# Kernel optimization log

Hardware: AMD Instinct MI355X
Metric: run time of the kernel (lower is better)

The kernel has to match this reference:

```python
import jax, jax.numpy as jnp
import numpy as np

BATCH, SEQ, FEAT, UNITS, OUT = 128, 2048, 64, 64, 6


def setup_inputs() -> dict:
    key = jax.random.key(0)
    ks = jax.random.split(key, 12)
    s = 0.05
    inp = {
        "x": jax.random.normal(ks[0], (BATCH, SEQ, FEAT), dtype=jnp.float32),
        # LSTMCell 0 (kernel, recurrent_kernel, bias); gate order i,f,g,o
        "W0": jax.random.normal(ks[1], (FEAT, 4 * UNITS), dtype=jnp.float32) * s,
        "U0": jax.random.normal(ks[2], (UNITS, 4 * UNITS), dtype=jnp.float32) * s,
        "b0": jax.random.normal(ks[3], (4 * UNITS,), dtype=jnp.float32) * s,
        # LSTMCell 1 (shared by layers 2 AND 3, as in the original code)
        "W1": jax.random.normal(ks[4], (UNITS, 4 * UNITS), dtype=jnp.float32) * s,
        "U1": jax.random.normal(ks[5], (UNITS, 4 * UNITS), dtype=jnp.float32) * s,
        "b1": jax.random.normal(ks[6], (4 * UNITS,), dtype=jnp.float32) * s,
        # Dense heads
        "Wf": jax.random.normal(ks[7], (UNITS, 64), dtype=jnp.float32) * s,
        "bf": jax.random.normal(ks[8], (64,), dtype=jnp.float32) * s,
        "Wo": jax.random.normal(ks[9], (64, OUT), dtype=jnp.float32) * s,
        "bo": jax.random.normal(ks[10], (OUT,), dtype=jnp.float32) * s,
    }
    return inp


def _lstm_cell(c, h, xin, W, U, b):
    # Keras LSTMCell math, gate order i, f, g(candidate), o
    z = xin @ W + h @ U + b  # [B, 4U]
    i, f, g, o = jnp.split(z, 4, axis=-1)
    c_new = jax.nn.sigmoid(f) * c + jax.nn.sigmoid(i) * jnp.tanh(g)
    h_new = jax.nn.sigmoid(o) * jnp.tanh(c_new)
    return c_new, h_new


def reference(x, W0, U0, b0, W1, U1, b1, Wf, bf, Wo, bo):
    B = x.shape[0]
    z = jnp.zeros((B, UNITS), dtype=x.dtype)
    init = (z, z, z, z, z, z)  # (c0,h0,c1,h1,c2,h2)

    def step(carry, xt):
        c0, h0, c1, h1, c2, h2 = carry
        c0, h0 = _lstm_cell(c0, h0, xt, W0, U0, b0)
        c1, h1 = _lstm_cell(c1, h1, h0, W1, U1, b1)
        # NOTE: original code reuses rnn_cell1's weights for the 3rd layer
        c2, h2 = _lstm_cell(c2, h2, h1, W1, U1, b1)
        return (c0, h0, c1, h1, c2, h2), None

    xt = jnp.swapaxes(x, 0, 1)  # [T, B, F]
    (c0, h0, c1, h1, c2, h2), _ = jax.lax.scan(step, init, xt)
    y = jax.nn.relu(h2 @ Wf + bf)
    return y @ Wo + bo
```

## Files before the change

### kernel.cpp

```cpp
#include <hip/hip_runtime.h>

#define BATCHN 128
#define SEQT   2048
#define FEAT   64
#define UNITS  64
#define NCOL   256
#define OUTD   6

typedef __fp16 hv2 __attribute__((ext_vector_type(2)));

__device__ __forceinline__ float fast_exp2(float x) {
#if __has_builtin(__builtin_amdgcn_exp2f)
    return __builtin_amdgcn_exp2f(x);
#else
    return exp2f(x);
#endif
}
__device__ __forceinline__ float fast_rcp(float x) {
#if __has_builtin(__builtin_amdgcn_rcpf)
    return __builtin_amdgcn_rcpf(x);
#else
    return 1.0f / x;
#endif
}
__device__ __forceinline__ float sig_(float x) {
    return fast_rcp(1.0f + fast_exp2(-1.4426950408889634f * x));
}
__device__ __forceinline__ float tanh_(float x) {
    float e = fast_exp2(-2.8853900817779268f * x);
    return fmaf(2.0f, fast_rcp(1.0f + e), -1.0f);
}

__device__ __forceinline__ float fdot2_(hv2 a, hv2 b, float c) {
#if __has_builtin(__builtin_amdgcn_fdot2)
    return __builtin_amdgcn_fdot2(a, b, c, false);
#else
    return fmaf((float)a.x, (float)b.x, fmaf((float)a.y, (float)b.y, c));
#endif
}
__device__ __forceinline__ hv2 cvtpk_(float a, float b) {
    return __builtin_amdgcn_cvt_pkrtz(a, b);
}
__device__ __forceinline__ unsigned int rlane_(unsigned int v, int l) {
    return (unsigned int)__builtin_amdgcn_readlane((int)v, l);
}
__device__ __forceinline__ float bperm_(int byteaddr, float v) {
    return __builtin_bit_cast(float,
        __builtin_amdgcn_ds_bpermute(byteaddr, __builtin_bit_cast(int, v)));
}

__global__ __launch_bounds__(384, 1)
void lstm3_ffrec2(const float* __restrict__ x,
                  const float* __restrict__ W0, const float* __restrict__ U0,
                  const float* __restrict__ b0,
                  const float* __restrict__ W1, const float* __restrict__ U1,
                  const float* __restrict__ b1,
                  const float* __restrict__ Wf, const float* __restrict__ bfv,
                  const float* __restrict__ Wo, const float* __restrict__ bov,
                  float* __restrict__ out)
{
    const int b   = blockIdx.x;
    const int tid = threadIdx.x;
    const int wid = tid >> 6;
    const int g   = wid >> 1;
    const int r   = wid & 1;
    const int u   = tid & 63;
    const int j32 = u & 31;

    __shared__ unsigned int lhp[3][2][32];
    __shared__ __align__(16) float lzf[3][2][UNITS][4];
    __shared__ float lh2f[UNITS];
    __shared__ float lact[UNITS];

    const float* M = (g == 0) ? ((r == 0) ? W0 : U0) : ((r == 0) ? W1 : U1);
    const float* bsel = (g == 0) ? b0 : b1;

    hv2 wM[32][4];
    float biasv[4];
#pragma unroll
    for (int gg = 0; gg < 4; ++gg) {
        const int col = (gg << 6) + u;
#pragma unroll
        for (int j = 0; j < 32; ++j) {
            hv2 w;
            w.x = (__fp16)M[(2 * j) * NCOL + col];
            w.y = (__fp16)M[(2 * j + 1) * NCOL + col];
            wM[j][gg] = w;
        }
        biasv[gg] = bsel[col];
    }

    if (tid < 192) ((unsigned int*)lhp)[tid] = 0u;
    for (int i = tid; i < 3 * 2 * UNITS * 4; i += 384) ((float*)lzf)[i] = 0.f;

    const float2* x2 = (const float2*)(x + (size_t)b * SEQT * FEAT);
    float2 xrA = {0.f, 0.f}, xrB = {0.f, 0.f};
    if (wid == 0 && u < 32) {
        xrA = x2[0 * 32 + u];
        xrB = x2[1 * 32 + u];
    }
    __syncthreads();

    const int alpha = 2 * g + r;
    float c = 0.f, h = 0.f;
    unsigned int rpk = 0u;

#define TICK(TK, XR)                                                          \
    {                                                                         \
        const int t_ = (TK) - alpha;                                          \
        const float2 xcur = XR;                                               \
        if (wid == 0 && u < 32) {                    \
            int tn = (TK) + 2; if (tn > SEQT - 1) tn = SEQT - 1;              \
            XR = x2[(size_t)tn * 32 + u];                                     \
        }                                                                     \
        if (t_ >= 0 && t_ < SEQT) {                                           \
            const int p_ = t_ & 1;                                            \
            unsigned int srcpk;                                               \
            float4 zin = {0.f, 0.f, 0.f, 0.f};                                \
            if (r == 0) {                                                     \
                srcpk = (g == 0) ? __builtin_bit_cast(unsigned int,           \
                                                      cvtpk_(xcur.x, xcur.y)) \
                                 : lhp[g - 1][p_][j32];            \
            } else {                                                          \
                srcpk = rpk;                                                  \
                zin = *(const float4*)&lzf[g][p_][u][0];     \
            }                                                                 \
            float aA0 = 0.f, aA1 = 0.f, aA2 = 0.f, aA3 = 0.f;                 \
            float aB0 = 0.f, aB1 = 0.f, aB2 = 0.f, aB3 = 0.f;                 \
            _Pragma("unroll")                                                 \
            for (int j = 0; j < 32; j += 2) {                                 \
                hv2 p0 = __builtin_bit_cast(hv2, rlane_(srcpk, j));           \
                hv2 p1 = __builtin_bit_cast(hv2, rlane_(srcpk, j + 1));       \
                aA0 = fdot2_(p0, wM[j][0], aA0);                              \
                aA1 = fdot2_(p0, wM[j][1], aA1);                              \
                aA2 = fdot2_(p0, wM[j][2], aA2);                              \
                aA3 = fdot2_(p0, wM[j][3], aA3);                              \
                aB0 = fdot2_(p1, wM[j + 1][0], aB0);                          \
                aB1 = fdot2_(p1, wM[j + 1][1], aB1);                          \
                aB2 = fdot2_(p1, wM[j + 1][2], aB2);                          \
                aB3 = fdot2_(p1, wM[j + 1][3], aB3);                          \
            }                                                                 \
            if (r == 0) {                   \
                float4 z4 = {aA0 + aB0 + biasv[0], aA1 + aB1 + biasv[1],      \
                             aA2 + aB2 + biasv[2], aA3 + aB3 + biasv[3]};     \
                *(float4*)&lzf[g][p_][u][0] = z4;                             \
            } else {                       \
                const float zi = aA0 + aB0 + zin.x;                           \
                const float zf = aA1 + aB1 + zin.y;                           \
                const float zg = aA2 + aB2 + zin.z;                           \
                const float zo = aA3 + aB3 + zin.w;                           \
                const float ig = sig_(zi), fg = sig_(zf);                     \
                const float gv = tanh_(zg), og = sig_(zo);                    \
                c = fg * c + ig * gv;                                         \
                h = og * tanh_(c);                                            \
                const float h0 = bperm_(j32 * 8,     h);                      \
                const float h1 = bperm_(j32 * 8 + 4, h);                      \
                rpk = __builtin_bit_cast(unsigned int, cvtpk_(h0, h1));       \
                if (u < 32) lhp[g][p_][u] = rpk;                              \
                if (g == 2 && t_ == SEQT - 1) lh2f[u] = h;                    \
            }                                                                 \
        }                                                                     \
        asm volatile("s_waitcnt lgkmcnt(0)\n\ts_barrier" ::: "memory");       \
    }

    for (int tk = 0; tk < SEQT + 6; tk += 2) {
        TICK(tk,     xrA)
        TICK(tk + 1, xrB)
    }
#undef TICK

    __syncthreads();

    if (tid < UNITS) {
        float a = bfv[tid];
#pragma unroll
        for (int k = 0; k < UNITS; ++k) a += lh2f[k] * Wf[k * 64 + tid];
        lact[tid] = fmaxf(a, 0.f);
    }
    __syncthreads();
    if (tid < OUTD) {
        float a = bov[tid];
#pragma unroll
        for (int k = 0; k < UNITS; ++k) a += lact[k] * Wo[k * OUTD + tid];
        out[b * OUTD + tid] = a;
    }
}

extern "C" void kernel_launch(void* const* d_in, const int* in_sizes, int n_in,
                              void* d_out, int out_size, void* d_ws, size_t ws_size,
                              hipStream_t stream) {
    const float* x   = (const float*)d_in[0];
    const float* W0  = (const float*)d_in[1];
    const float* U0  = (const float*)d_in[2];
    const float* b0  = (const float*)d_in[3];
    const float* W1  = (const float*)d_in[4];
    const float* U1  = (const float*)d_in[5];
    const float* b1  = (const float*)d_in[6];
    const float* Wf  = (const float*)d_in[7];
    const float* bfv = (const float*)d_in[8];
    const float* Wo  = (const float*)d_in[9];
    const float* bov = (const float*)d_in[10];
    float* out = (float*)d_out;

    lstm3_ffrec2<<<BATCHN, 384, 0, stream>>>(x, W0, U0, b0, W1, U1, b1,
                                             Wf, bfv, Wo, bov, out);
}
```

Baseline: 1.898 ms.

## Process two timesteps per pipeline tick to halve block barriers

Restructures the wavefront-pipelined LSTM so each tick advances two consecutive timesteps instead of one. This halves the number of workgroup barriers and LDS handoffs. Input-projection waves now compute two projections per tick into double-buffered LDS slots. Recurrent waves run two dependent cell updates back-to-back, using direct readlane of fp32 h for the inner step. The trade-off is a longer serial critical path per tick on the recurrent waves and extra readlane/pack instructions.

```diff
diff --git a/kernel.cpp b/kernel.cpp
--- a/kernel.cpp
+++ b/kernel.cpp
@@ -6,6 +6,7 @@
 #define UNITS  64
 #define NCOL   256
 #define OUTD   6
+#define NTICK  1030
 
 typedef __fp16 hv2 __attribute__((ext_vector_type(2)));
 
@@ -44,20 +45,27 @@
 __device__ __forceinline__ unsigned int rlane_(unsigned int v, int l) {
     return (unsigned int)__builtin_amdgcn_readlane((int)v, l);
 }
+__device__ __forceinline__ float rlf_(float v, int l) {
+    return __builtin_bit_cast(float,
+        __builtin_amdgcn_readlane(__builtin_bit_cast(int, v), l));
+}
 __device__ __forceinline__ float bperm_(int byteaddr, float v) {
     return __builtin_bit_cast(float,
         __builtin_amdgcn_ds_bpermute(byteaddr, __builtin_bit_cast(int, v)));
 }
+__device__ __forceinline__ unsigned int pku_(hv2 v) {
+    return __builtin_bit_cast(unsigned int, v);
+}
 
 __global__ __launch_bounds__(384, 1)
-void lstm3_ffrec2(const float* __restrict__ x,
-                  const float* __restrict__ W0, const float* __restrict__ U0,
-                  const float* __restrict__ b0,
-                  const float* __restrict__ W1, const float* __restrict__ U1,
-                  const float* __restrict__ b1,
-                  const float* __restrict__ Wf, const float* __restrict__ bfv,
-                  const float* __restrict__ Wo, const float* __restrict__ bov,
-                  float* __restrict__ out)
+void lstm3_2step(const float* __restrict__ x,
+                 const float* __restrict__ W0, const float* __restrict__ U0,
+                 const float* __restrict__ b0,
+                 const float* __restrict__ W1, const float* __restrict__ U1,
+                 const float* __restrict__ b1,
+                 const float* __restrict__ Wf, const float* __restrict__ bfv,
+                 const float* __restrict__ Wo, const float* __restrict__ bov,
+                 float* __restrict__ out)
 {
     const int b   = blockIdx.x;
     const int tid = threadIdx.x;
@@ -67,8 +75,8 @@
     const int u   = tid & 63;
     const int j32 = u & 31;
 
-    __shared__ unsigned int lhp[3][2][32];
-    __shared__ __align__(16) float lzf[3][2][UNITS][4];
+    __shared__ unsigned int lhp[3][2][2][32];
+    __shared__ __align__(16) float lzf[3][2][2][UNITS][4];
     __shared__ float lh2f[UNITS];
     __shared__ float lact[UNITS];
 
@@ -90,84 +98,135 @@
         biasv[gg] = bsel[col];
     }
 
-    if (tid < 192) ((unsigned int*)lhp)[tid] = 0u;
-    for (int i = tid; i < 3 * 2 * UNITS * 4; i += 384) ((float*)lzf)[i] = 0.f;
+    if (tid < 384) ((unsigned int*)lhp)[tid] = 0u;
+    for (int i = tid; i < 3 * 2 * 2 * UNITS * 4; i += 384) ((float*)lzf)[i] = 0.f;
 
     const float2* x2 = (const float2*)(x + (size_t)b * SEQT * FEAT);
-    float2 xrA = {0.f, 0.f}, xrB = {0.f, 0.f};
+    float2 xA0 = {0.f,0.f}, xA1 = {0.f,0.f}, xB0 = {0.f,0.f}, xB1 = {0.f,0.f};
     if (wid == 0 && u < 32) {
-        xrA = x2[0 * 32 + u];
-        xrB = x2[1 * 32 + u];
+        xA0 = x2[0 * 32 + u];  xA1 = x2[1 * 32 + u];
+        xB0 = x2[2 * 32 + u];  xB1 = x2[3 * 32 + u];
     }
     __syncthreads();
 
     const int alpha = 2 * g + r;
-    float c = 0.f, h = 0.f;
+    float c = 0.f;
     unsigned int rpk = 0u;
 
-#define TICK(TK, XR)                                                          \
-    {                                                                         \
-        const int t_ = (TK) - alpha;                                          \
-        const float2 xcur = XR;                                               \
-        if (wid == 0 && u < 32) {                    \
-            int tn = (TK) + 2; if (tn > SEQT - 1) tn = SEQT - 1;              \
-            XR = x2[(size_t)tn * 32 + u];                                     \
-        }                                                                     \
-        if (t_ >= 0 && t_ < SEQT) {                                           \
-            const int p_ = t_ & 1;                                            \
-            unsigned int srcpk;                                               \
-            float4 zin = {0.f, 0.f, 0.f, 0.f};                                \
+#define DOT_PK(SRC, S0, S1, S2, S3)                                           \
+    {                                                                         \
+        float dA0=0.f,dA1=0.f,dA2=0.f,dA3=0.f,dB0=0.f,dB1=0.f,dB2=0.f,dB3=0.f;\
+        _Pragma("unroll")                                                     \
+        for (int j = 0; j < 32; j += 2) {                                     \
+            hv2 p0 = __builtin_bit_cast(hv2, rlane_(SRC, j));                 \
+            hv2 p1 = __builtin_bit_cast(hv2, rlane_(SRC, j + 1));             \
+            dA0 = fdot2_(p0, wM[j][0], dA0);                                  \
+            dA1 = fdot2_(p0, wM[j][1], dA1);                                  \
+            dA2 = fdot2_(p0, wM[j][2], dA2);                                  \
+            dA3 = fdot2_(p0, wM[j][3], dA3);                                  \
+            dB0 = fdot2_(p1, wM[j + 1][0], dB0);                              \
+            dB1 = fdot2_(p1, wM[j + 1][1], dB1);                              \
+            dB2 = fdot2_(p1, wM[j + 1][2], dB2);                              \
+            dB3 = fdot2_(p1, wM[j + 1][3], dB3);                              \
+        }                                                                     \
+        S0 = dA0 + dB0; S1 = dA1 + dB1; S2 = dA2 + dB2; S3 = dA3 + dB3;       \
+    }
+
+#define DOT_H(HV, S0, S1, S2, S3)                                             \
+    {                                                                         \
+        float dA0=0.f,dA1=0.f,dA2=0.f,dA3=0.f,dB0=0.f,dB1=0.f,dB2=0.f,dB3=0.f;\
+        _Pragma("unroll")                                                     \
+        for (int j = 0; j < 32; j += 2) {                                     \
+            hv2 p0 = cvtpk_(rlf_(HV, 2 * j),     rlf_(HV, 2 * j + 1));        \
+            hv2 p1 = cvtpk_(rlf_(HV, 2 * j + 2), rlf_(HV, 2 * j + 3));        \
+            dA0 = fdot2_(p0, wM[j][0], dA0);                                  \
+            dA1 = fdot2_(p0, wM[j][1], dA1);                                  \
+            dA2 = fdot2_(p0, wM[j][2], dA2);                                  \
+            dA3 = fdot2_(p0, wM[j][3], dA3);                                  \
+            dB0 = fdot2_(p1, wM[j + 1][0], dB0);                              \
+            dB1 = fdot2_(p1, wM[j + 1][1], dB1);                              \
+            dB2 = fdot2_(p1, wM[j + 1][2], dB2);                              \
+            dB3 = fdot2_(p1, wM[j + 1][3], dB3);                              \
+        }                                                                     \
+        S0 = dA0 + dB0; S1 = dA1 + dB1; S2 = dA2 + dB2; S3 = dA3 + dB3;       \
+    }
+
+#define GATES(Z0, Z1, Z2, Z3, HOUT)                                           \
+    {                                                                         \
+        const float ig = sig_(Z0), fg = sig_(Z1);                             \
+        const float gv = tanh_(Z2), og = sig_(Z3);                            \
+        c = fg * c + ig * gv;                                                 \
+        HOUT = og * tanh_(c);                                                 \
+    }
+
+#define TICK(TK, X0, X1)                                                      \
+    {                                                                         \
+        const int t0_ = 2 * ((TK) - alpha);                                   \
+        const float2 xc0 = X0, xc1 = X1;                                      \
+        if (wid == 0 && u < 32) {        \
+            int tn = 2 * ((TK) + 2);                                          \
+            if (tn > SEQT - 2) tn = SEQT - 2;                                 \
+            X0 = x2[(size_t)tn * 32 + u];                                     \
+            X1 = x2[(size_t)(tn + 1) * 32 + u];                               \
+        }                                                                     \
+        if (t0_ >= 0 && t0_ < SEQT) {                                         \
+            const int q_ = (TK) & 1;                                          \
             if (r == 0) {                                                     \
-                srcpk = (g == 0) ? __builtin_bit_cast(unsigned int,           \
-                                                      cvtpk_(xcur.x, xcur.y)) \
-                                 : lhp[g - 1][p_][j32];            \
+                unsigned int fp0, fp1;                                        \
+                if (g == 0) {                                                 \
+                    fp0 = pku_(cvtpk_(xc0.x, xc0.y));                         \
+                    fp1 = pku_(cvtpk_(xc1.x, xc1.y));                         \
+                } else {                                                      \
+                    fp0 = lhp[g - 1][q_ ^ 1][0][j32];                         \
+                    fp1 = lhp[g - 1][q_ ^ 1][1][j32];                         \
+                }                                                             \
+                float s0, s1, s2, s3;                                         \
+                DOT_PK(fp0, s0, s1, s2, s3)                                   \
+                {                                                             \
+                    float4 z4 = {s0 + biasv[0], s1 + biasv[1],                \
+                                 s2 + biasv[2], s3 + biasv[3]};               \
+                    *(float4*)&lzf[g][q_][0][u][0] = z4;                      \
+                }                                                             \
+                DOT_PK(fp1, s0, s1, s2, s3)                                   \
+                {                                                             \
+                    float4 z4 = {s0 + biasv[0], s1 + biasv[1],                \
+                                 s2 + biasv[2], s3 + biasv[3]};               \
+                    *(float4*)&lzf[g][q_][1][u][0] = z4;                      \
+                }                                                             \
             } else {                                                          \
-                srcpk = rpk;                                                  \
-                zin = *(const float4*)&lzf[g][p_][u][0];     \
+                float4 zin0 = *(const float4*)&lzf[g][q_ ^ 1][0][u][0];       \
+                float4 zin1 = *(const float4*)&lzf[g][q_ ^ 1][1][u][0];       \
+                float s0, s1, s2, s3, h0v, h1v;                               \
+                DOT_PK(rpk, s0, s1, s2, s3)                                   \
+                GATES(s0 + zin0.x, s1 + zin0.y, s2 + zin0.z, s3 + zin0.w, h0v)\
+                DOT_H(h0v, s0, s1, s2, s3)                                    \
+                GATES(s0 + zin1.x, s1 + zin1.y, s2 + zin1.z, s3 + zin1.w, h1v)\
+                {     \
+                    const float pa = bperm_(j32 * 8,     h0v);                \
+                    const float pb = bperm_(j32 * 8 + 4, h0v);                \
+                    const unsigned int pk0 = pku_(cvtpk_(pa, pb));            \
+                    const float pc = bperm_(j32 * 8,     h1v);                \
+                    const float pd = bperm_(j32 * 8 + 4, h1v);                \
+                    rpk = pku_(cvtpk_(pc, pd));                               \
+                    if (u < 32) {                                             \
+                        lhp[g][q_][0][u] = pk0;                               \
+                        lhp[g][q_][1][u] = rpk;                               \
+                    }                                                         \
+                }                                                             \
+                if (g == 2 && t0_ == SEQT - 2) lh2f[u] = h1v;                 \
             }                                                                 \
-            float aA0 = 0.f, aA1 = 0.f, aA2 = 0.f, aA3 = 0.f;                 \
-            float aB0 = 0.f, aB1 = 0.f, aB2 = 0.f, aB3 = 0.f;                 \
-            _Pragma("unroll")                                                 \
-            for (int j = 0; j < 32; j += 2) {                                 \
-                hv2 p0 = __builtin_bit_cast(hv2, rlane_(srcpk, j));           \
-                hv2 p1 = __builtin_bit_cast(hv2, rlane_(srcpk, j + 1));       \
-                aA0 = fdot2_(p0, wM[j][0], aA0);                              \
-                aA1 = fdot2_(p0, wM[j][1], aA1);                              \
-                aA2 = fdot2_(p0, wM[j][2], aA2);                              \
-                aA3 = fdot2_(p0, wM[j][3], aA3);                              \
-                aB0 = fdot2_(p1, wM[j + 1][0], aB0);                          \
-                aB1 = fdot2_(p1, wM[j + 1][1], aB1);                          \
-                aB2 = fdot2_(p1, wM[j + 1][2], aB2);                          \
-                aB3 = fdot2_(p1, wM[j + 1][3], aB3);                          \
-            }                                                                 \
-            if (r == 0) {                   \
-                float4 z4 = {aA0 + aB0 + biasv[0], aA1 + aB1 + biasv[1],      \
-                             aA2 + aB2 + biasv[2], aA3 + aB3 + biasv[3]};     \
-                *(float4*)&lzf[g][p_][u][0] = z4;                             \
-            } else {                       \
-                const float zi = aA0 + aB0 + zin.x;                           \
-                const float zf = aA1 + aB1 + zin.y;                           \
-                const float zg = aA2 + aB2 + zin.z;                           \
-                const float zo = aA3 + aB3 + zin.w;                           \
-                const float ig = sig_(zi), fg = sig_(zf);                     \
-                const float gv = tanh_(zg), og = sig_(zo);                    \
-                c = fg * c + ig * gv;                                         \
-                h = og * tanh_(c);                                            \
-                const float h0 = bperm_(j32 * 8,     h);                      \
-                const float h1 = bperm_(j32 * 8 + 4, h);                      \
-                rpk = __builtin_bit_cast(unsigned int, cvtpk_(h0, h1));       \
-                if (u < 32) lhp[g][p_][u] = rpk;                              \
-                if (g == 2 && t_ == SEQT - 1) lh2f[u] = h;                    \
-            }                                                                 \
         }                                                                     \
         asm volatile("s_waitcnt lgkmcnt(0)\n\ts_barrier" ::: "memory");       \
     }
 
-    for (int tk = 0; tk < SEQT + 6; tk += 2) {
-        TICK(tk,     xrA)
-        TICK(tk + 1, xrB)
+    for (int tk = 0; tk < NTICK; tk += 2) {
+        TICK(tk,     xA0, xA1)
+        TICK(tk + 1, xB0, xB1)
     }
 #undef TICK
+#undef GATES
+#undef DOT_H
+#undef DOT_PK
 
     __syncthreads();
 
@@ -202,6 +261,6 @@
     const float* bov = (const float*)d_in[10];
     float* out = (float*)d_out;
 
-    lstm3_ffrec2<<<BATCHN, 384, 0, stream>>>(x, W0, U0, b0, W1, U1, b1,
-                                             Wf, bfv, Wo, bov, out);
-}
+    lstm3_2step<<<BATCHN, 384, 0, stream>>>(x, W0, U0, b0, W1, U1, b1,
+                                            Wf, bfv, Wo, bov, out);
+}
```

Result: slower. 2.008 ms (+5.8%).
